# Optimization experiments

Measured on AMD Instinct MI355X. Metric: run time of the kernel, lower is better.

Reference implementation:

```python
import jax, jax.numpy as jnp
import numpy as np

D = 2048          # input_dim == dec_hidden_size
S = 16384         # src_time_steps
H = 250           # projection hidden (hard-coded in module)


def setup_inputs() -> dict:
    key = jax.random.key(0)
    ks = jax.random.split(key, 12)
    sc_d = 1.0 / np.sqrt(D)
    sc_3d = 1.0 / np.sqrt(3 * D)
    sc_h = 1.0 / np.sqrt(H)
    return {
        "s_prev": jax.random.normal(ks[0], (1, 1, D), jnp.float32),
        "enc_hs": jax.random.normal(ks[1], (1, S, D), jnp.float32),
        "cur_men_rep": jax.random.normal(ks[2], (1, 1, D), jnp.float32),
        "src_mask": jax.random.randint(ks[3], (1, S), 0, 2, jnp.int32),
        "W_info": jax.random.normal(ks[4], (D, D), jnp.float32) * sc_d,
        "W_ctx": jax.random.normal(ks[5], (D, D), jnp.float32) * sc_d,
        "W_q": jax.random.normal(ks[6], (D, D), jnp.float32) * sc_d,
        "b_q": jnp.zeros((D,), jnp.float32),
        "W_p1": jax.random.normal(ks[7], (H, 3 * D), jnp.float32) * sc_3d,
        "b_p1": jnp.zeros((H,), jnp.float32),
        "W_p2": jax.random.normal(ks[8], (1, H), jnp.float32) * sc_h,
        "b_p2": jnp.zeros((1,), jnp.float32),
    }


def reference(s_prev, enc_hs, cur_men_rep, src_mask,
              W_info, W_ctx, W_q, b_q, W_p1, b_p1, W_p2, b_p2):
    # dh = linear_info(cur_men_rep): [1,1,D]; uh = linear_ctx(enc_hs): [1,S,D]
    dh = jnp.einsum('bqe,de->bqd', cur_men_rep, W_info)
    uh = jnp.einsum('bse,de->bsd', enc_hs, W_ctx)
    wq = jnp.einsum('bqe,de->bqd', s_prev, W_q) + b_q
    # cat(uh, wq.repeat, dh.repeat) -> tanh : [1,S,3D]
    wquh = jnp.tanh(jnp.concatenate(
        [uh, jnp.broadcast_to(wq, uh.shape), jnp.broadcast_to(dh, uh.shape)],
        axis=2))
    # projection: Linear(3D,250) -> Dropout(eval: identity) -> ReLU -> Linear(250,1)
    h = jax.nn.relu(jnp.einsum('bsk,hk->bsh', wquh, W_p1) + b_p1)
    scores = (jnp.einsum('bsh,oh->bso', h, W_p2) + b_p2).squeeze()   # [S] (B=1)
    scores = jnp.where(src_mask.squeeze().astype(bool), -jnp.inf, scores)
    attn = jax.nn.softmax(scores, axis=-1)                            # [S]
    ctx = jnp.sum(enc_hs * attn[None, :, None], axis=1)               # [1,D]
    return attn, ctx
```

## Files before the change

kernel.cpp:

```cpp
#include <hip/hip_runtime.h>
#include <hip/hip_bf16.h>
#include <stdint.h>

#define DD 2048
#define SS 16384
#define HH 250
#define GEMMB_GRID 264

typedef __attribute__((ext_vector_type(8))) short bf16x8;
typedef __attribute__((ext_vector_type(4))) short bf16x4;
typedef __attribute__((ext_vector_type(4))) float f32x4;

__device__ __forceinline__ unsigned short f2bf(float f){
  union { float f; uint32_t u; } v; v.f = f;
  uint32_t u = v.u;
  return (unsigned short)((u + 0x7fffu + ((u >> 16) & 1u)) >> 16);
}
__device__ __forceinline__ float bf2f(unsigned short h){
  union { uint32_t u; float f; } v; v.u = ((uint32_t)h) << 16; return v.f;
}
__device__ __forceinline__ bf16x4 pk4(float4 a){
  bf16x4 v;
  v[0]=(short)f2bf(a.x); v[1]=(short)f2bf(a.y); v[2]=(short)f2bf(a.z); v[3]=(short)f2bf(a.w);
  return v;
}
__device__ __forceinline__ float fast_tanh(float x){
  return 1.0f - 2.0f / (1.0f + __expf(2.0f * x));
}
__device__ __forceinline__ void gl_lds16(const void* g, void* l){
  __builtin_amdgcn_global_load_lds((const __attribute__((address_space(1))) void*)g,
                                   (__attribute__((address_space(3))) void*)l, 16, 0, 0);
}

__global__ __launch_bounds__(256) void prep_kernel(
    const float* __restrict__ s_prev, const float* __restrict__ cmr,
    const float* __restrict__ Wq, const float* __restrict__ bq,
    const float* __restrict__ Winfo,
    float* __restrict__ twq, float* __restrict__ tdh,
    const int* __restrict__ mask, int* __restrict__ idx, int* __restrict__ cpos,
    int* __restrict__ mcount)
{
  const int b = blockIdx.x, t = threadIdx.x;
  if(b < 1024){
    int wid = t >> 6, lane = t & 63;
    bool isq = b < 512;
    int r = (isq ? b : b - 512) * 4 + wid;
    const float* M = (isq ? Wq : Winfo) + (size_t)r * DD;
    const float* x = isq ? s_prev : cmr;
    float s = 0.f;
    for(int i = lane; i < DD; i += 64) s += M[i] * x[i];
    #pragma unroll
    for(int o = 32; o; o >>= 1) s += __shfl_xor(s, o);
    if(lane == 0){
      if(isq) twq[r] = fast_tanh(s + bq[r]);
      else    tdh[r] = fast_tanh(s);
    }
  } else {
    __shared__ int wsum[4];
    const int lane = t & 63, w = t >> 6;
    int running = 0;
    for(int k = 0; k < 64; k++){
      const int e = k * 256 + t;
      const int m = (mask[e] == 0);
      unsigned long long bal = __ballot(m);
      if(lane == 0) wsum[w] = __popcll(bal);
      __syncthreads();
      int wpre = 0;
      #pragma unroll
      for(int i = 0; i < 4; i++) if(i < w) wpre += wsum[i];
      int tot = wsum[0] + wsum[1] + wsum[2] + wsum[3];
      const int lpre = __popcll(bal & ((1ull << lane) - 1ull));
      const int pos = running + wpre + lpre;
      if(m){ idx[pos] = e; cpos[e] = pos; } else cpos[e] = -1;
      running += tot;
      __syncthreads();
    }
    if(t == 0){
      mcount[0] = running;
      mcount[1] = (running + 255) & ~255;
      mcount[2] = (running + 63) & ~63;
    }
  }
}

__global__ __launch_bounds__(256) void conv_kernel(
    const float* __restrict__ enc, const int* __restrict__ idx,
    const int* __restrict__ mcount, unsigned short* __restrict__ encb,
    const float* __restrict__ W_ctx, unsigned short* __restrict__ wctxb,
    const float* __restrict__ W_p1, unsigned short* __restrict__ wp1ab,
    const float* __restrict__ bp1,
    const float* __restrict__ twq, const float* __restrict__ tdh,
    float* __restrict__ bias2)
{
  const int b = blockIdx.x, t = threadIdx.x;
  if(b < 2048){
    const int mc0 = mcount[0], mc1 = mcount[1];
    #pragma unroll
    for(int r = 0; r < 8; r++){
      int j = b * 8 + r;
      if(j >= mc1) return;
      unsigned short* o = encb + (size_t)j * DD + t * 8;
      if(j >= mc0){
        bf16x8 z;
        #pragma unroll
        for(int i = 0; i < 8; i++) z[i] = 0;
        *(bf16x8*)o = z;
      } else {
        const float4* p = (const float4*)(enc + (size_t)idx[j] * DD + t * 8);
        float4 a = p[0], c = p[1];
        bf16x8 v;
        v[0]=(short)f2bf(a.x); v[1]=(short)f2bf(a.y); v[2]=(short)f2bf(a.z); v[3]=(short)f2bf(a.w);
        v[4]=(short)f2bf(c.x); v[5]=(short)f2bf(c.y); v[6]=(short)f2bf(c.z); v[7]=(short)f2bf(c.w);
        *(bf16x8*)o = v;
      }
    }
  } else if(b < 2112){
    int h = (b - 2048) * 4 + (t >> 6);
    int lane = t & 63;
    if(h >= HH){ if(lane == 0 && h < 256) bias2[h] = 0.f; return; }
    const float* r1 = W_p1 + (size_t)h * (3 * DD) + DD;
    const float* r2 = W_p1 + (size_t)h * (3 * DD) + 2 * DD;
    float s = 0.f;
    for(int i = lane; i < DD; i += 64) s += r1[i] * twq[i] + r2[i] * tdh[i];
    #pragma unroll
    for(int o = 32; o; o >>= 1) s += __shfl_xor(s, o);
    if(lane == 0) bias2[h] = s + bp1[h];
  } else if(b < 2368){
    const float4* in4 = (const float4*)W_ctx;
    bf16x4* out4 = (bf16x4*)wctxb;
    const int gt = (b - 2112) * 256 + t;
    for(int i = gt; i < 1048576; i += 65536) out4[i] = pk4(in4[i]);
  } else {
    bf16x4* out4 = (bf16x4*)wp1ab;
    const int gt = (b - 2368) * 256 + t;
    #pragma unroll
    for(int k = 0; k < 16; k++){
      int i = gt + k * 8192;
      int row = i >> 9, col = i & 511;
      bf16x4 v;
      if(row < HH){
        v = pk4(*(const float4*)(W_p1 + (size_t)row * (3 * DD) + (col << 2)));
      } else {
        v[0] = 0; v[1] = 0; v[2] = 0; v[3] = 0;
      }
      out4[i] = v;
    }
  }
}

__device__ __forceinline__ void stage_half(const unsigned short* __restrict__ g,
                                           int grow0, int kt, char* ldsbase,
                                           int wid, int lane)
{
  const int srow = lane >> 3;
  const int c = (lane & 7) ^ srow;
  #pragma unroll
  for(int i = 0; i < 2; i++){
    int r8 = (wid * 2 + i) * 8;
    gl_lds16(g + (size_t)(grow0 + r8 + srow) * DD + kt + c * 8,
             ldsbase + r8 * 128);
  }
}
#define RDF(base, lr, kc) (*(const bf16x8*)((base) + (lr) * 128 + (((kc) * 16) ^ (((lr) & 7) << 4))))

__global__ __launch_bounds__(512, 2) void gemmA_kernel(
    const unsigned short* __restrict__ A, const unsigned short* __restrict__ B,
    const int* __restrict__ mcount, unsigned short* __restrict__ Ct)
{
  __shared__ alignas(128) char lds[131072];
  const int tid = threadIdx.x, lane = tid & 63, wid = tid >> 6;
  const int wm = wid >> 2, wn = wid & 3;
  const int slot = blockIdx.x >> 3;
  const int mt = (blockIdx.x & 7) + ((slot >> 3) << 3);
  const int n0 = (slot & 7) * 256;
  const int MT = mcount[1] >> 8;
  if(mt >= MT) return;
  const int m0 = mt * 256;
  const int frow = lane & 15, kch = lane >> 4;

  f32x4 acc[8][4] = {};

  stage_half(A, m0,        0, lds,                 wid, lane);
  stage_half(A, m0 + 128,  0, lds + 16384,         wid, lane);
  stage_half(B, n0,        0, lds + 32768,         wid, lane);
  stage_half(B, n0 + 128,  0, lds + 49152,         wid, lane);
  stage_half(B, n0,       64, lds + 65536 + 32768, wid, lane);
  stage_half(B, n0 + 128, 64, lds + 65536 + 49152, wid, lane);
  asm volatile("s_waitcnt vmcnt(4)" ::: "memory");
  __builtin_amdgcn_s_barrier();

  #pragma unroll 2
  for(int t = 0; t < 32; t++){
    const int d = t & 1;
    char* Ab = lds + d * 65536;
    char* Bb = Ab + 32768;
    char* An = lds + (d ^ 1) * 65536;
    bf16x8 bfr[4][2];
    #pragma unroll
    for(int q = 0; q < 4; q++){
      if(q == 0){
        #pragma unroll
        for(int nr = 0; nr < 4; nr++){
          int row = wn * 64 + nr * 16 + frow;
          #pragma unroll
          for(int ks = 0; ks < 2; ks++) bfr[nr][ks] = RDF(Bb, row, ks * 4 + kch);
        }
      }
      bf16x8 afr[2][2];
      #pragma unroll
      for(int mi = 0; mi < 2; mi++){
        int row = wm * 128 + (q * 2 + mi) * 16 + frow;
        #pragma unroll
        for(int ks = 0; ks < 2; ks++) afr[mi][ks] = RDF(Ab, row, ks * 4 + kch);
      }
      if(q == 0){
        if(t + 1 < 32){
          stage_half(A, m0,       (t + 1) * 64, An,         wid, lane);
          stage_half(A, m0 + 128, (t + 1) * 64, An + 16384, wid, lane);
        }
      } else if(q == 1){
        if(t + 2 < 32) stage_half(B, n0,       (t + 2) * 64, Bb,         wid, lane);
      } else if(q == 2){
        if(t + 2 < 32) stage_half(B, n0 + 128, (t + 2) * 64, Bb + 16384, wid, lane);
      }
      __builtin_amdgcn_s_barrier();
      __builtin_amdgcn_sched_barrier(0);
      __builtin_amdgcn_s_setprio(1);
      #pragma unroll
      for(int mi = 0; mi < 2; mi++)
        #pragma unroll
        for(int nr = 0; nr < 4; nr++)
          #pragma unroll
          for(int ks = 0; ks < 2; ks++)
            acc[q * 2 + mi][nr] = __builtin_amdgcn_mfma_f32_16x16x32_bf16(
                afr[mi][ks], bfr[nr][ks], acc[q * 2 + mi][nr], 0, 0, 0);
      __builtin_amdgcn_s_setprio(0);
      __builtin_amdgcn_sched_barrier(0);
      if(q == 3){
        if(t < 30)       asm volatile("s_waitcnt vmcnt(4)" ::: "memory");
        else if(t == 30) asm volatile("s_waitcnt vmcnt(0)" ::: "memory");
      }
      __builtin_amdgcn_s_barrier();
    }
  }

  const int r0 = m0 + wm * 128 + (lane >> 4) * 4;
  const int c0 = n0 + wn * 64 + frow;
  #pragma unroll
  for(int mr = 0; mr < 8; mr++)
    #pragma unroll
    for(int nr = 0; nr < 4; nr++)
      #pragma unroll
      for(int r = 0; r < 4; r++)
        Ct[(size_t)(r0 + mr * 16 + r) * DD + c0 + nr * 16] = f2bf(fast_tanh(acc[mr][nr][r]));
}

__global__ __launch_bounds__(512, 4) void gemmB_kernel(
    const unsigned short* __restrict__ A, const unsigned short* __restrict__ B,
    const int* __restrict__ mcount, const float* __restrict__ bias2,
    const float* __restrict__ w2, const float* __restrict__ bp2,
    float* __restrict__ attnc, float* __restrict__ Tpart)
{
  __shared__ alignas(128) char lds[81920];
  __shared__ float sred[8][32];
  const int tid = threadIdx.x, lane = tid & 63, wid = tid >> 6;
  const int wm = wid >> 2, wn = wid & 3;
  const int m0 = blockIdx.x * 64;
  const int mc0 = mcount[0], mc2 = mcount[2];
  if(m0 >= mc2){ if(tid == 0) Tpart[blockIdx.x] = 0.f; return; }
  const int frow = lane & 15, kch = lane >> 4;
  const int srow = lane >> 3, sc = ((lane & 7) ^ srow) * 8;

  f32x4 acc[2][4] = {};

  gl_lds16(A + (size_t)(m0 + wid * 8 + srow) * DD + sc, lds + wid * 1024);
  #pragma unroll
  for(int i = 0; i < 4; i++){
    int l = wid + 8 * i;
    gl_lds16(B + (size_t)(l * 8 + srow) * DD + sc,      lds + 16384 + l * 1024);
    gl_lds16(B + (size_t)(l * 8 + srow) * DD + 64 + sc, lds + 49152 + l * 1024);
  }
  asm volatile("s_waitcnt vmcnt(4)" ::: "memory");
  __builtin_amdgcn_s_barrier();

  #pragma unroll 2
  for(int t = 0; t < 32; t++){
    const int d = t & 1;
    char* Ab = lds + d * 8192;
    char* An = lds + (d ^ 1) * 8192;
    char* Bb = lds + 16384 + d * 32768;
    bf16x8 bfr[4][2], afr[2];
    #pragma unroll
    for(int q = 0; q < 2; q++){
      if(q == 0){
        #pragma unroll
        for(int nr = 0; nr < 4; nr++){
          int row = wn * 64 + nr * 16 + frow;
          #pragma unroll
          for(int ks = 0; ks < 2; ks++) bfr[nr][ks] = RDF(Bb, row, ks * 4 + kch);
        }
      }
      {
        int row = wm * 32 + q * 16 + frow;
        #pragma unroll
        for(int ks = 0; ks < 2; ks++) afr[ks] = RDF(Ab, row, ks * 4 + kch);
      }
      if(q == 0){
        if(t + 1 < 32)
          gl_lds16(A + (size_t)(m0 + wid * 8 + srow) * DD + (t + 1) * 64 + sc, An + wid * 1024);
      } else {
        if(t + 2 < 32){
          #pragma unroll
          for(int i = 0; i < 4; i++){
            int l = wid + 8 * i;
            gl_lds16(B + (size_t)(l * 8 + srow) * DD + (t + 2) * 64 + sc, Bb + l * 1024);
          }
        }
      }
      __builtin_amdgcn_s_barrier();
      __builtin_amdgcn_sched_barrier(0);
      __builtin_amdgcn_s_setprio(1);
      #pragma unroll
      for(int nr = 0; nr < 4; nr++)
        #pragma unroll
        for(int ks = 0; ks < 2; ks++)
          acc[q][nr] = __builtin_amdgcn_mfma_f32_16x16x32_bf16(afr[ks], bfr[nr][ks], acc[q][nr], 0, 0, 0);
      __builtin_amdgcn_s_setprio(0);
      __builtin_amdgcn_sched_barrier(0);
      if(q == 1){
        if(t < 30)       asm volatile("s_waitcnt vmcnt(4)" ::: "memory");
        else if(t == 30) asm volatile("s_waitcnt vmcnt(0)" ::: "memory");
      }
      __builtin_amdgcn_s_barrier();
    }
  }

  float w2v[4], b2v[4];
  #pragma unroll
  for(int in = 0; in < 4; in++){
    int n = wn * 64 + in * 16 + frow;
    w2v[in] = (n < HH) ? w2[n] : 0.f;
    b2v[in] = bias2[n];
  }
  #pragma unroll
  for(int mi = 0; mi < 2; mi++){
    #pragma unroll
    for(int r = 0; r < 4; r++){
      float s = 0.f;
      #pragma unroll
      for(int in = 0; in < 4; in++){
        float h = acc[mi][in][r] + b2v[in];
        s += (h > 0.f ? h : 0.f) * w2v[in];
      }
      s += __shfl_xor(s, 1); s += __shfl_xor(s, 2);
      s += __shfl_xor(s, 4); s += __shfl_xor(s, 8);
      if(frow == 0) sred[wid][mi * 16 + (lane >> 4) * 4 + r] = s;
    }
  }
  __syncthreads();
  if(tid < 64){
    int wmr = tid >> 5, rr = tid & 31;
    float s = sred[wmr * 4][rr] + sred[wmr * 4 + 1][rr] + sred[wmr * 4 + 2][rr]
            + sred[wmr * 4 + 3][rr] + bp2[0];
    int j = m0 + tid;
    float e = (j < mc0) ? __expf(s) : 0.f;
    if(j < mc0) attnc[j] = e;
    #pragma unroll
    for(int o = 32; o; o >>= 1) e += __shfl_xor(e, o);
    if(tid == 0) Tpart[blockIdx.x] = e;
  }
}

__global__ __launch_bounds__(256) void normctx_kernel(
    const float* __restrict__ attnc, const int* __restrict__ cpos,
    const int* __restrict__ mcount, const float* __restrict__ Tpart,
    const unsigned short* __restrict__ encb,
    float* __restrict__ out, float* __restrict__ part)
{
  const int b = blockIdx.x, t = threadIdx.x;
  if(b < 64){
    __shared__ float sT;
    if(t == 0){
      float s = 0.f;
      for(int i = 0; i < GEMMB_GRID; i++) s += Tpart[i];
      sT = 1.0f / s;
    }
    __syncthreads();
    int i = b * 256 + t;
    int cp = cpos[i];
    out[i] = (cp >= 0) ? attnc[cp] * sT : 0.f;
  } else {
    const int bb = b - 64;
    const int mc0 = mcount[0];
    const int chunk = (mc0 + 255) >> 8;
    const int j0 = bb * chunk;
    const int j1 = min(j0 + chunk, mc0);
    float a[8] = {};
    for(int j = j0; j < j1; j++){
      float e = attnc[j];
      bf16x8 v = *(const bf16x8*)(encb + (size_t)j * DD + t * 8);
      #pragma unroll
      for(int k = 0; k < 8; k++) a[k] += e * bf2f((unsigned short)v[k]);
    }
    float* o = part + (size_t)bb * DD + t * 8;
    #pragma unroll
    for(int k = 0; k < 8; k++) o[k] = a[k];
  }
}

__global__ __launch_bounds__(256) void ctxr_kernel(
    const float* __restrict__ part, const float* __restrict__ Tpart,
    float* __restrict__ out)
{
  __shared__ float sT;
  if(threadIdx.x == 0){
    float s = 0.f;
    for(int i = 0; i < GEMMB_GRID; i++) s += Tpart[i];
    sT = 1.0f / s;
  }
  __syncthreads();
  const int dcol = blockIdx.x * 256 + threadIdx.x;
  float s = 0.f;
  for(int b = 0; b < 256; b++) s += part[(size_t)b * DD + dcol];
  out[dcol] = s * sT;
}

extern "C" void kernel_launch(void* const* d_in, const int* in_sizes, int n_in,
                              void* d_out, int out_size, void* d_ws, size_t ws_size,
                              hipStream_t stream)
{
  const float* s_prev = (const float*)d_in[0];
  const float* enc    = (const float*)d_in[1];
  const float* cmr    = (const float*)d_in[2];
  const int*   mask   = (const int*)d_in[3];
  const float* W_info = (const float*)d_in[4];
  const float* W_ctx  = (const float*)d_in[5];
  const float* W_q    = (const float*)d_in[6];
  const float* b_q    = (const float*)d_in[7];
  const float* W_p1   = (const float*)d_in[8];
  const float* b_p1   = (const float*)d_in[9];
  const float* W_p2   = (const float*)d_in[10];
  const float* b_p2   = (const float*)d_in[11];
  float* out = (float*)d_out;

  char* ws = (char*)d_ws;
  unsigned short* encb    = (unsigned short*)(ws);
  unsigned short* tanhbuf = (unsigned short*)(ws + 67108864);
  unsigned short* wctxb   = (unsigned short*)(ws + 134217728);
  unsigned short* wp1ab   = (unsigned short*)(ws + 142606336);
  int*   idx    = (int*)(ws + 143654912);
  int*   cpos   = (int*)(ws + 143720448);
  float* attnc  = (float*)(ws + 143785984);
  float* part   = (float*)(ws + 143851520);
  float* twq    = (float*)(ws + 145948672);
  float* tdh    = (float*)(ws + 145956864);
  float* bias2  = (float*)(ws + 145965056);
  int*   mcount = (int*)(ws + 145966080);
  float* Tpart  = (float*)(ws + 145966208);

  prep_kernel<<<1025, 256, 0, stream>>>(s_prev, cmr, W_q, b_q, W_info,
                                        twq, tdh, mask, idx, cpos, mcount);
  conv_kernel<<<2400, 256, 0, stream>>>(enc, idx, mcount, encb,
                                        W_ctx, wctxb, W_p1, wp1ab,
                                        b_p1, twq, tdh, bias2);
  gemmA_kernel<<<512, 512, 0, stream>>>(encb, wctxb, mcount, tanhbuf);
  gemmB_kernel<<<GEMMB_GRID, 512, 0, stream>>>(tanhbuf, wp1ab, mcount, bias2,
                                               W_p2, b_p2, attnc, Tpart);
  normctx_kernel<<<320, 256, 0, stream>>>(attnc, cpos, mcount, Tpart,
                                          encb, out, part);
  ctxr_kernel<<<8, 256, 0, stream>>>(part, Tpart, out + SS);
}
```

Baseline: 178.7 us.

## Split gemmA into 256x256 main tiles plus 64-row tail blocks

The GEMM over unmasked encoder rows now handles the first 8192 rows with the 256x256 tiled path in 256 blocks. Any rows beyond 8192 go to 32 extra blocks that use a smaller 64x256 tile and loop over row strips. The launch grid shrinks from 512 to 288 blocks, with the aim of balancing the ragged tail across CUs instead of running a partial second wave of large tiles. The tail blocks have lower MFMA reuse per loaded byte and process their strips serially.

```diff
diff --git a/kernel.cpp b/kernel.cpp
--- a/kernel.cpp
+++ b/kernel.cpp
@@ -169,90 +169,180 @@
 {
   __shared__ alignas(128) char lds[131072];
   const int tid = threadIdx.x, lane = tid & 63, wid = tid >> 6;
+  const int frow = lane & 15, kch = lane >> 4;
+  const int srow = lane >> 3;
+  const int sc = ((lane & 7) ^ srow) * 8;
+
+  if(blockIdx.x < 256){
+    const int wm = wid >> 2, wn = wid & 3;
+    const int slot = blockIdx.x >> 3;
+    const int mt = (blockIdx.x & 7) + ((slot >> 3) << 3);
+    const int n0 = (slot & 7) * 256;
+    const int MT = mcount[1] >> 8;
+    if(mt >= MT || mt >= 32) return;
+    const int m0 = mt * 256;
+
+    f32x4 acc[8][4] = {};
+
+    stage_half(A, m0,        0, lds,                 wid, lane);
+    stage_half(A, m0 + 128,  0, lds + 16384,         wid, lane);
+    stage_half(B, n0,        0, lds + 32768,         wid, lane);
+    stage_half(B, n0 + 128,  0, lds + 49152,         wid, lane);
+    stage_half(B, n0,       64, lds + 65536 + 32768, wid, lane);
+    stage_half(B, n0 + 128, 64, lds + 65536 + 49152, wid, lane);
+    asm volatile("s_waitcnt vmcnt(4)" ::: "memory");
+    __builtin_amdgcn_s_barrier();
+
+    #pragma unroll 2
+    for(int t = 0; t < 32; t++){
+      const int d = t & 1;
+      char* Ab = lds + d * 65536;
+      char* Bb = Ab + 32768;
+      char* An = lds + (d ^ 1) * 65536;
+      bf16x8 bfr[4][2];
+      #pragma unroll
+      for(int q = 0; q < 4; q++){
+        if(q == 0){
+          #pragma unroll
+          for(int nr = 0; nr < 4; nr++){
+            int row = wn * 64 + nr * 16 + frow;
+            #pragma unroll
+            for(int ks = 0; ks < 2; ks++) bfr[nr][ks] = RDF(Bb, row, ks * 4 + kch);
+          }
+        }
+        bf16x8 afr[2][2];
+        #pragma unroll
+        for(int mi = 0; mi < 2; mi++){
+          int row = wm * 128 + (q * 2 + mi) * 16 + frow;
+          #pragma unroll
+          for(int ks = 0; ks < 2; ks++) afr[mi][ks] = RDF(Ab, row, ks * 4 + kch);
+        }
+        if(q == 0){
+          if(t + 1 < 32){
+            stage_half(A, m0,       (t + 1) * 64, An,         wid, lane);
+            stage_half(A, m0 + 128, (t + 1) * 64, An + 16384, wid, lane);
+          }
+        } else if(q == 1){
+          if(t + 2 < 32) stage_half(B, n0,       (t + 2) * 64, Bb,         wid, lane);
+        } else if(q == 2){
+          if(t + 2 < 32) stage_half(B, n0 + 128, (t + 2) * 64, Bb + 16384, wid, lane);
+        }
+        __builtin_amdgcn_s_barrier();
+        __builtin_amdgcn_sched_barrier(0);
+        __builtin_amdgcn_s_setprio(1);
+        #pragma unroll
+        for(int mi = 0; mi < 2; mi++)
+          #pragma unroll
+          for(int nr = 0; nr < 4; nr++)
+            #pragma unroll
+            for(int ks = 0; ks < 2; ks++)
+              acc[q * 2 + mi][nr] = __builtin_amdgcn_mfma_f32_16x16x32_bf16(
+                  afr[mi][ks], bfr[nr][ks], acc[q * 2 + mi][nr], 0, 0, 0);
+        __builtin_amdgcn_s_setprio(0);
+        __builtin_amdgcn_sched_barrier(0);
+        if(q == 3){
+          if(t < 30)       asm volatile("s_waitcnt vmcnt(4)" ::: "memory");
+          else if(t == 30) asm volatile("s_waitcnt vmcnt(0)" ::: "memory");
+        }
+        __builtin_amdgcn_s_barrier();
+      }
+    }
+
+    const int r0 = m0 + wm * 128 + (lane >> 4) * 4;
+    const int c0 = n0 + wn * 64 + frow;
+    #pragma unroll
+    for(int mr = 0; mr < 8; mr++)
+      #pragma unroll
+      for(int nr = 0; nr < 4; nr++)
+        #pragma unroll
+        for(int r = 0; r < 4; r++)
+          Ct[(size_t)(r0 + mr * 16 + r) * DD + c0 + nr * 16] = f2bf(fast_tanh(acc[mr][nr][r]));
+    return;
+  }
+
+  const int mc1 = mcount[1];
+  if(mc1 <= 8192) return;
+  const int tb = blockIdx.x - 256;
+  const int n0t = (tb & 7) * 256;
   const int wm = wid >> 2, wn = wid & 3;
-  const int slot = blockIdx.x >> 3;
-  const int mt = (blockIdx.x & 7) + ((slot >> 3) << 3);
-  const int n0 = (slot & 7) * 256;
-  const int MT = mcount[1] >> 8;
-  if(mt >= MT) return;
-  const int m0 = mt * 256;
-  const int frow = lane & 15, kch = lane >> 4;
-
-  f32x4 acc[8][4] = {};
-
-  stage_half(A, m0,        0, lds,                 wid, lane);
-  stage_half(A, m0 + 128,  0, lds + 16384,         wid, lane);
-  stage_half(B, n0,        0, lds + 32768,         wid, lane);
-  stage_half(B, n0 + 128,  0, lds + 49152,         wid, lane);
-  stage_half(B, n0,       64, lds + 65536 + 32768, wid, lane);
-  stage_half(B, n0 + 128, 64, lds + 65536 + 49152, wid, lane);
-  asm volatile("s_waitcnt vmcnt(4)" ::: "memory");
-  __builtin_amdgcn_s_barrier();
-
-  #pragma unroll 2
-  for(int t = 0; t < 32; t++){
-    const int d = t & 1;
-    char* Ab = lds + d * 65536;
-    char* Bb = Ab + 32768;
-    char* An = lds + (d ^ 1) * 65536;
-    bf16x8 bfr[4][2];
-    #pragma unroll
-    for(int q = 0; q < 4; q++){
-      if(q == 0){
-        #pragma unroll
-        for(int nr = 0; nr < 4; nr++){
-          int row = wn * 64 + nr * 16 + frow;
-          #pragma unroll
-          for(int ks = 0; ks < 2; ks++) bfr[nr][ks] = RDF(Bb, row, ks * 4 + kch);
-        }
-      }
-      bf16x8 afr[2][2];
-      #pragma unroll
-      for(int mi = 0; mi < 2; mi++){
-        int row = wm * 128 + (q * 2 + mi) * 16 + frow;
-        #pragma unroll
-        for(int ks = 0; ks < 2; ks++) afr[mi][ks] = RDF(Ab, row, ks * 4 + kch);
-      }
-      if(q == 0){
-        if(t + 1 < 32){
-          stage_half(A, m0,       (t + 1) * 64, An,         wid, lane);
-          stage_half(A, m0 + 128, (t + 1) * 64, An + 16384, wid, lane);
-        }
-      } else if(q == 1){
-        if(t + 2 < 32) stage_half(B, n0,       (t + 2) * 64, Bb,         wid, lane);
-      } else if(q == 2){
-        if(t + 2 < 32) stage_half(B, n0 + 128, (t + 2) * 64, Bb + 16384, wid, lane);
-      }
-      __builtin_amdgcn_s_barrier();
-      __builtin_amdgcn_sched_barrier(0);
-      __builtin_amdgcn_s_setprio(1);
-      #pragma unroll
-      for(int mi = 0; mi < 2; mi++)
+
+  for(int ms = (tb >> 3); 8192 + ms * 64 < mc1; ms += 4){
+    const int m0t = 8192 + ms * 64;
+    f32x4 acc2[2][4] = {};
+
+    gl_lds16(A + (size_t)(m0t + wid * 8 + srow) * DD + sc, lds + wid * 1024);
+    #pragma unroll
+    for(int i = 0; i < 4; i++){
+      int l = wid + 8 * i;
+      gl_lds16(B + (size_t)(n0t + l * 8 + srow) * DD + sc,      lds + 16384 + l * 1024);
+      gl_lds16(B + (size_t)(n0t + l * 8 + srow) * DD + 64 + sc, lds + 49152 + l * 1024);
+    }
+    asm volatile("s_waitcnt vmcnt(4)" ::: "memory");
+    __builtin_amdgcn_s_barrier();
+
+    #pragma unroll 2
+    for(int t = 0; t < 32; t++){
+      const int d = t & 1;
+      char* Ab = lds + d * 8192;
+      char* An = lds + (d ^ 1) * 8192;
+      char* Bb = lds + 16384 + d * 32768;
+      bf16x8 bfr[4][2], afr[2];
+      #pragma unroll
+      for(int q = 0; q < 2; q++){
+        if(q == 0){
+          #pragma unroll
+          for(int nr = 0; nr < 4; nr++){
+            int row = wn * 64 + nr * 16 + frow;
+            #pragma unroll
+            for(int ks = 0; ks < 2; ks++) bfr[nr][ks] = RDF(Bb, row, ks * 4 + kch);
+          }
+        }
+        {
+          int row = wm * 32 + q * 16 + frow;
+          #pragma unroll
+          for(int ks = 0; ks < 2; ks++) afr[ks] = RDF(Ab, row, ks * 4 + kch);
+        }
+        if(q == 0){
+          if(t + 1 < 32)
+            gl_lds16(A + (size_t)(m0t + wid * 8 + srow) * DD + (t + 1) * 64 + sc, An + wid * 1024);
+        } else {
+          if(t + 2 < 32){
+            #pragma unroll
+            for(int i = 0; i < 4; i++){
+              int l = wid + 8 * i;
+              gl_lds16(B + (size_t)(n0t + l * 8 + srow) * DD + (t + 2) * 64 + sc, Bb + l * 1024);
+            }
+          }
+        }
+        __builtin_amdgcn_s_barrier();
+        __builtin_amdgcn_sched_barrier(0);
+        __builtin_amdgcn_s_setprio(1);
         #pragma unroll
         for(int nr = 0; nr < 4; nr++)
           #pragma unroll
           for(int ks = 0; ks < 2; ks++)
-            acc[q * 2 + mi][nr] = __builtin_amdgcn_mfma_f32_16x16x32_bf16(
-                afr[mi][ks], bfr[nr][ks], acc[q * 2 + mi][nr], 0, 0, 0);
-      __builtin_amdgcn_s_setprio(0);
-      __builtin_amdgcn_sched_barrier(0);
-      if(q == 3){
-        if(t < 30)       asm volatile("s_waitcnt vmcnt(4)" ::: "memory");
-        else if(t == 30) asm volatile("s_waitcnt vmcnt(0)" ::: "memory");
-      }
-      __builtin_amdgcn_s_barrier();
-    }
-  }
-
-  const int r0 = m0 + wm * 128 + (lane >> 4) * 4;
-  const int c0 = n0 + wn * 64 + frow;
-  #pragma unroll
-  for(int mr = 0; mr < 8; mr++)
-    #pragma unroll
-    for(int nr = 0; nr < 4; nr++)
-      #pragma unroll
-      for(int r = 0; r < 4; r++)
-        Ct[(size_t)(r0 + mr * 16 + r) * DD + c0 + nr * 16] = f2bf(fast_tanh(acc[mr][nr][r]));
+            acc2[q][nr] = __builtin_amdgcn_mfma_f32_16x16x32_bf16(afr[ks], bfr[nr][ks], acc2[q][nr], 0, 0, 0);
+        __builtin_amdgcn_s_setprio(0);
+        __builtin_amdgcn_sched_barrier(0);
+        if(q == 1){
+          if(t < 30)       asm volatile("s_waitcnt vmcnt(4)" ::: "memory");
+          else if(t == 30) asm volatile("s_waitcnt vmcnt(0)" ::: "memory");
+        }
+        __builtin_amdgcn_s_barrier();
+      }
+    }
+
+    const int r0t = m0t + wm * 32 + (lane >> 4) * 4;
+    const int c0t = n0t + wn * 64 + frow;
+    #pragma unroll
+    for(int mi = 0; mi < 2; mi++)
+      #pragma unroll
+      for(int in = 0; in < 4; in++)
+        #pragma unroll
+        for(int r = 0; r < 4; r++)
+          Ct[(size_t)(r0t + mi * 16 + r) * DD + c0t + in * 16] = f2bf(fast_tanh(acc2[mi][in][r]));
+    __builtin_amdgcn_s_barrier();
+  }
 }
 
 __global__ __launch_bounds__(512, 4) void gemmB_kernel(
@@ -463,7 +553,7 @@
   conv_kernel<<<2400, 256, 0, stream>>>(enc, idx, mcount, encb,
                                         W_ctx, wctxb, W_p1, wp1ab,
                                         b_p1, twq, tdh, bias2);
-  gemmA_kernel<<<512, 512, 0, stream>>>(encb, wctxb, mcount, tanhbuf);
+  gemmA_kernel<<<288, 512, 0, stream>>>(encb, wctxb, mcount, tanhbuf);
   gemmB_kernel<<<GEMMB_GRID, 512, 0, stream>>>(tanhbuf, wp1ab, mcount, bias2,
                                                W_p2, b_p2, attnc, Tpart);
   normctx_kernel<<<320, 256, 0, stream>>>(attnc, cpos, mcount, Tpart,
```

New measurement: 178.2 us, median of 2. No clear change (-0.3%).
